# Performance work log

Hardware: AMD Instinct MI355X
Metric: run time of the kernel (lower is better)

Reference implementation:

```python
import jax, jax.numpy as jnp
import numpy as np

DIM = 512
HEADS = 8
HEAD_DIM = DIM // HEADS
SCALE = DIM ** (-0.5)  # note: original uses full dim, not head_dim


def setup_inputs() -> dict:
    key = jax.random.key(0)
    ks = jax.random.split(key, 7)
    B, N = 4, 2048
    x = jax.random.normal(ks[0], (B, N, DIM), dtype=jnp.float32)
    A_phi = jax.random.normal(ks[1], (B, N, N), dtype=jnp.float32)
    # parameters (torch Linear: y = x @ W.T + b)
    w_qkv = jax.random.normal(ks[2], (3 * DIM, DIM), dtype=jnp.float32) * (DIM ** -0.5)
    b_qkv = jax.random.normal(ks[3], (3 * DIM,), dtype=jnp.float32) * 0.02
    w_out = jax.random.normal(ks[4], (DIM, DIM), dtype=jnp.float32) * (DIM ** -0.5)
    b_out = jax.random.normal(ks[5], (DIM,), dtype=jnp.float32) * 0.02
    gamma = jnp.array(1.0, dtype=jnp.float32)
    return {"x": x, "A_phi": A_phi, "w_qkv": w_qkv, "b_qkv": b_qkv,
            "w_out": w_out, "b_out": b_out, "gamma": gamma}


def reference(x, A_phi, w_qkv, b_qkv, w_out, b_out, gamma):
    B, N, D = x.shape
    qkv = x @ w_qkv.T + b_qkv  # [B,N,3D]
    q, k, v = jnp.split(qkv, 3, axis=-1)
    def to_heads(t):
        return t.reshape(B, N, HEADS, HEAD_DIM).transpose(0, 2, 1, 3)  # [B,H,N,d]
    q, k, v = to_heads(q), to_heads(k), to_heads(v)
    attn = jnp.einsum('bhqd,bhkd->bhqk', q, k) * SCALE
    attn = attn + gamma * A_phi[:, None, :, :]
    attn = jax.nn.softmax(attn, axis=-1)
    out = jnp.einsum('bhqk,bhkd->bhqd', attn, v)
    out = out.transpose(0, 2, 1, 3).reshape(B, N, D)
    return out @ w_out.T + b_out
```

## Files before the change

### kernel.cpp

```cpp
#include <hip/hip_runtime.h>

#define NSEQ 2048
#define SCALE 0.04419417382415922f
#define LOG2E 1.44269504088896f

typedef __attribute__((ext_vector_type(8))) short short8v;
typedef __attribute__((ext_vector_type(4))) float f32x4;

#define GLOAD_LDS16(g, l) __builtin_amdgcn_global_load_lds( \
    (const __attribute__((address_space(1))) void*)(g),     \
    (__attribute__((address_space(3))) void*)(l), 16, 0, 0)

__device__ __forceinline__ unsigned short f2bf(float f) {
    unsigned int u = __builtin_bit_cast(unsigned int, f);
    u += 0x7fff + ((u >> 16) & 1);
    return (unsigned short)(u >> 16);
}

__device__ __forceinline__ float exp2_fast(float x) {
    float r; asm("v_exp_f32 %0, %1" : "=v"(r) : "v"(x)); return r;
}

__device__ __forceinline__ unsigned int pack_bf16_rh(float a, float b) {
    unsigned int ua = __builtin_bit_cast(unsigned int, a) + 0x8000u;
    unsigned int ub = __builtin_bit_cast(unsigned int, b) + 0x8000u;
    return __builtin_amdgcn_perm(ub, ua, 0x07060302u);
}

__global__ __launch_bounds__(256) void cvt_all(
    const float* __restrict__ x, const float* __restrict__ wq,
    const float* __restrict__ wo,
    unsigned short* __restrict__ xb, unsigned short* __restrict__ wqb,
    unsigned short* __restrict__ wob)
{
    int bid = blockIdx.x;
    const float* in;
    unsigned short* out;
    int i;
    if (bid < 4096)      { in = x;  out = xb;  i = bid * 256 + threadIdx.x; }
    else if (bid < 4864) { in = wq; out = wqb; i = (bid - 4096) * 256 + threadIdx.x; }
    else                 { in = wo; out = wob; i = (bid - 4864) * 256 + threadIdx.x; }
    float4 v = ((const float4*)in)[i];
    ushort4 o;
    o.x = f2bf(v.x); o.y = f2bf(v.y); o.z = f2bf(v.z); o.w = f2bf(v.w);
    ((ushort4*)out)[i] = o;
}

template<int MODE, int BM, int BN, int NX, int NWG>
__global__ __launch_bounds__(256) void gemm_bf16(
    const unsigned short* __restrict__ A,
    const unsigned short* __restrict__ W,
    const float* __restrict__ bias,
    unsigned short* __restrict__ Qws,
    unsigned short* __restrict__ Kws,
    unsigned short* __restrict__ Vtws,
    float* __restrict__ Cout)
{
    const int WM = BM / 2, WN = BN / 2;
    __shared__ __attribute__((aligned(16))) unsigned short As[BM * 64];
    __shared__ __attribute__((aligned(16))) unsigned short Bs[BN * 64];

    int tid = threadIdx.x;
    int lane = tid & 63, w = tid >> 6;
    int wm = w >> 1, wn = w & 1;
    int g = lane >> 4, fr = lane & 15;

    int id = blockIdx.x + NX * blockIdx.y;
    int wgid = (id & 7) * (NWG / 8) + (id >> 3);
    int m0 = (wgid / NX) * BM, n0 = (wgid % NX) * BN;

    f32x4 acc[WM / 16][4] = {};

    for (int k0 = 0; k0 < 512; k0 += 64) {
        __syncthreads();
#pragma unroll
        for (int c = 0; c < BM * 8 / 256; ++c) {
            int chunk = tid + c * 256;
            int row = chunk >> 3, c8 = chunk & 7;
            int gcol = (c8 ^ (row & 7)) * 8;
            GLOAD_LDS16(A + (size_t)(m0 + row) * 512 + k0 + gcol, &As[chunk * 8]);
        }
#pragma unroll
        for (int c = 0; c < BN * 8 / 256; ++c) {
            int chunk = tid + c * 256;
            int row = chunk >> 3, c8 = chunk & 7;
            int gcol = (c8 ^ (row & 7)) * 8;
            GLOAD_LDS16(W + (size_t)(n0 + row) * 512 + k0 + gcol, &Bs[chunk * 8]);
        }
        __syncthreads();
#pragma unroll
        for (int kk = 0; kk < 2; ++kk) {
            short8v af[WM / 16], bf[4];
#pragma unroll
            for (int mi = 0; mi < WM / 16; ++mi) {
                int row = wm * WM + mi * 16 + fr;
                af[mi] = *(const short8v*)(&As[row * 64 + (((kk * 4 + g) ^ (row & 7)) * 8)]);
            }
#pragma unroll
            for (int ni = 0; ni < 4; ++ni) {
                int row = wn * WN + ni * 16 + fr;
                bf[ni] = *(const short8v*)(&Bs[row * 64 + (((kk * 4 + g) ^ (row & 7)) * 8)]);
            }
#pragma unroll
            for (int mi = 0; mi < WM / 16; ++mi)
#pragma unroll
                for (int ni = 0; ni < 4; ++ni)
                    acc[mi][ni] = __builtin_amdgcn_mfma_f32_16x16x32_bf16(
                        af[mi], bf[ni], acc[mi][ni], 0, 0, 0);
        }
    }

#pragma unroll
    for (int mi = 0; mi < WM / 16; ++mi) {
#pragma unroll
        for (int ni = 0; ni < 4; ++ni) {
            int col = n0 + wn * WN + ni * 16 + fr;
            float bb = bias[col];
            int row0 = m0 + wm * WM + mi * 16 + g * 4;
            if (MODE == 0) {
                int b = row0 >> 11, s0 = row0 & 2047;
                if (col < 512) {
                    int h = col >> 6, d = col & 63;
#pragma unroll
                    for (int r = 0; r < 4; ++r)
                        Qws[(((size_t)(b * 8 + h) * NSEQ + s0 + r) << 6) + d] =
                            f2bf((acc[mi][ni][r] + bb) * (SCALE * LOG2E));
                } else if (col < 1024) {
                    int c2 = col - 512; int h = c2 >> 6, d = c2 & 63;
#pragma unroll
                    for (int r = 0; r < 4; ++r)
                        Kws[(((size_t)(b * 8 + h) * NSEQ + s0 + r) << 6) + d] =
                            f2bf(acc[mi][ni][r] + bb);
                } else {
                    int c2 = col - 1024; int h = c2 >> 6, d = c2 & 63;
                    uint2 pv;
                    pv.x = pack_bf16_rh(acc[mi][ni][0] + bb, acc[mi][ni][1] + bb);
                    pv.y = pack_bf16_rh(acc[mi][ni][2] + bb, acc[mi][ni][3] + bb);
                    *(uint2*)(&Vtws[((size_t)(b * 8 + h) * 64 + d) * NSEQ + s0]) = pv;
                }
            } else {
#pragma unroll
                for (int r = 0; r < 4; ++r)
                    Cout[(size_t)(row0 + r) * 512 + col] = acc[mi][ni][r] + bb;
            }
        }
    }
}

__global__ __launch_bounds__(512, 3) void attn_kernel(
    const unsigned short* __restrict__ Qws,
    const unsigned short* __restrict__ Kws,
    const unsigned short* __restrict__ Vtws,
    const float* __restrict__ A_phi,
    const float* __restrict__ gamma_p,
    unsigned short* __restrict__ Oout)
{
    __shared__ __attribute__((aligned(16))) unsigned short Ks[2][64 * 64];
    __shared__ __attribute__((aligned(16))) unsigned short Vts[2][64 * 64];
    __shared__ __attribute__((aligned(16))) unsigned short Pl[8][16 * 64];

    int tid = threadIdx.x, lane = tid & 63, w = tid >> 6;
    int g = lane >> 4, fr = lane & 15;

    int id = blockIdx.x;
    int b = (id & 7) >> 1, p = id & 1;
    int j = id >> 3;
    int h = j & 7;
    int qt = ((j >> 3) << 1) | p;
    int bh = b * 8 + h;
    int q0 = qt * 128 + w * 16;
    float g2 = gamma_p[0] * LOG2E;

    const unsigned short* Kb = Kws + (size_t)bh * NSEQ * 64;
    const unsigned short* Vb = Vtws + (size_t)bh * 64 * NSEQ;
    const float* Ap = A_phi + (size_t)b * NSEQ * NSEQ;

    short8v qf[2];
#pragma unroll
    for (int dc = 0; dc < 2; ++dc)
        qf[dc] = *(const short8v*)(Qws + ((size_t)bh * NSEQ + q0 + fr) * 64 + dc * 32 + g * 8);

    int c = tid;
    int krow = c >> 3;
    int kchunk = c & 7;
    int swK = (kchunk ^ ((krow >> 2) & 7)) * 8;
    int swV = (kchunk ^ (krow & 7)) * 8;
    int kcol = kchunk * 8;

    float l_lane[4] = {};
    f32x4 o_acc[4] = {};

    {
        short8v k0v = *(const short8v*)(Kb + c * 8);
        short8v v0v = *(const short8v*)(Vb + (size_t)krow * NSEQ + kcol);
        *(short8v*)(&Ks[0][krow * 64 + swK]) = k0v;
        *(short8v*)(&Vts[0][krow * 64 + swV]) = v0v;
    }
    __syncthreads();

    for (int kt = 0; kt < NSEQ / 64; ++kt) {
        int cur = kt & 1;

        short8v kreg, vreg;
        if (kt < NSEQ / 64 - 1) {
            kreg = *(const short8v*)(Kb + (kt + 1) * 4096 + c * 8);
            vreg = *(const short8v*)(Vb + (size_t)krow * NSEQ + (kt + 1) * 64 + kcol);
        }

        float4 av[4];
#pragma unroll
        for (int r = 0; r < 4; ++r)
            av[r] = *(const float4*)(Ap + (size_t)(q0 + g * 4 + r) * NSEQ + kt * 64 + 4 * fr);

        f32x4 sa[4] = {};
        __builtin_amdgcn_s_setprio(1);
#pragma unroll
        for (int kf = 0; kf < 4; ++kf) {
            int row = 4 * fr + kf;
#pragma unroll
            for (int dc = 0; dc < 2; ++dc) {
                short8v kfrag = *(const short8v*)(
                    &Ks[cur][row * 64 + (((dc * 4 + g) ^ ((row >> 2) & 7)) * 8)]);
                sa[kf] = __builtin_amdgcn_mfma_f32_16x16x32_bf16(qf[dc], kfrag, sa[kf], 0, 0, 0);
            }
        }
        __builtin_amdgcn_s_setprio(0);

#pragma unroll
        for (int r = 0; r < 4; ++r) {
            float e0 = exp2_fast(fmaf(g2, av[r].x, sa[0][r]));
            float e1 = exp2_fast(fmaf(g2, av[r].y, sa[1][r]));
            float e2 = exp2_fast(fmaf(g2, av[r].z, sa[2][r]));
            float e3 = exp2_fast(fmaf(g2, av[r].w, sa[3][r]));
            l_lane[r] += (e0 + e1) + (e2 + e3);
            int rp = g * 4 + r;
            uint2 pp;
            pp.x = pack_bf16_rh(e0, e1);
            pp.y = pack_bf16_rh(e2, e3);
            *(uint2*)(&Pl[w][rp * 64 + (((fr >> 1) ^ (rp & 7)) * 8) + (fr & 1) * 4]) = pp;
        }
        asm volatile("s_waitcnt lgkmcnt(0)" ::: "memory");

#pragma unroll
        for (int kc = 0; kc < 2; ++kc) {
            short8v pf = *(const short8v*)(
                &Pl[w][fr * 64 + (((kc * 4 + g) ^ (fr & 7)) * 8)]);
            __builtin_amdgcn_s_setprio(1);
#pragma unroll
            for (int nf = 0; nf < 4; ++nf) {
                int vrow = nf * 16 + fr;
                short8v vf = *(const short8v*)(
                    &Vts[cur][vrow * 64 + (((kc * 4 + g) ^ (vrow & 7)) * 8)]);
                o_acc[nf] = __builtin_amdgcn_mfma_f32_16x16x32_bf16(pf, vf, o_acc[nf], 0, 0, 0);
            }
            __builtin_amdgcn_s_setprio(0);
        }

        if (kt < NSEQ / 64 - 1) {
            *(short8v*)(&Ks[cur ^ 1][krow * 64 + swK]) = kreg;
            *(short8v*)(&Vts[cur ^ 1][krow * 64 + swV]) = vreg;
        }
        __syncthreads();
    }

#pragma unroll
    for (int r = 0; r < 4; ++r) {
        float l = l_lane[r];
        l += __shfl_xor(l, 1);
        l += __shfl_xor(l, 2);
        l += __shfl_xor(l, 4);
        l += __shfl_xor(l, 8);
        float inv = 1.0f / l;
        int qg = q0 + g * 4 + r;
#pragma unroll
        for (int nf = 0; nf < 4; ++nf)
            Oout[((size_t)b * NSEQ + qg) * 512 + h * 64 + nf * 16 + fr] =
                f2bf(o_acc[nf][r] * inv);
    }
}

extern "C" void kernel_launch(void* const* d_in, const int* in_sizes, int n_in,
                              void* d_out, int out_size, void* d_ws, size_t ws_size,
                              hipStream_t stream) {
    const float* x      = (const float*)d_in[0];
    const float* A_phi  = (const float*)d_in[1];
    const float* w_qkv  = (const float*)d_in[2];
    const float* b_qkv  = (const float*)d_in[3];
    const float* w_out  = (const float*)d_in[4];
    const float* b_out  = (const float*)d_in[5];
    const float* gamma  = (const float*)d_in[6];
    float* out = (float*)d_out;

    unsigned short* xb   = (unsigned short*)d_ws;
    unsigned short* wqb  = xb  + (size_t)8192 * 512;
    unsigned short* wob  = wqb + (size_t)1536 * 512;
    unsigned short* Qws  = wob + (size_t)512 * 512;
    unsigned short* Kws  = Qws + (size_t)4 * 8 * NSEQ * 64;
    unsigned short* Vtws = Kws + (size_t)4 * 8 * NSEQ * 64;
    unsigned short* Oat  = Vtws + (size_t)4 * 8 * NSEQ * 64;

    cvt_all<<<dim3(5120), dim3(256), 0, stream>>>(x, w_qkv, w_out, xb, wqb, wob);

    gemm_bf16<0, 128, 128, 12, 768><<<dim3(12, 64), dim3(256), 0, stream>>>(
        xb, wqb, b_qkv, Qws, Kws, Vtws, nullptr);

    attn_kernel<<<dim3(512), dim3(512), 0, stream>>>(
        Qws, Kws, Vtws, A_phi, gamma, Oat);

    gemm_bf16<1, 64, 128, 4, 512><<<dim3(4, 128), dim3(256), 0, stream>>>(
        Oat, wob, b_out, nullptr, nullptr, nullptr, out);
}
```

Measured before the change: 104.6 us.

## Split key range across two wave groups with 32-row query tiles per wave

```diff
diff --git a/kernel.cpp b/kernel.cpp
--- a/kernel.cpp
+++ b/kernel.cpp
@@ -147,7 +147,7 @@
     }
 }
 
-__global__ __launch_bounds__(512, 3) void attn_kernel(
+__global__ __launch_bounds__(512, 2) void attn_kernel(
     const unsigned short* __restrict__ Qws,
     const unsigned short* __restrict__ Kws,
     const unsigned short* __restrict__ Vtws,
@@ -155,12 +155,11 @@
     const float* __restrict__ gamma_p,
     unsigned short* __restrict__ Oout)
 {
-    __shared__ __attribute__((aligned(16))) unsigned short Ks[2][64 * 64];
-    __shared__ __attribute__((aligned(16))) unsigned short Vts[2][64 * 64];
-    __shared__ __attribute__((aligned(16))) unsigned short Pl[8][16 * 64];
+    __shared__ __attribute__((aligned(16))) unsigned short lds[32768];
 
     int tid = threadIdx.x, lane = tid & 63, w = tid >> 6;
     int g = lane >> 4, fr = lane & 15;
+    int G = w >> 2, wg = w & 3;
 
     int id = blockIdx.x;
     int b = (id & 7) >> 1, p = id & 1;
@@ -168,51 +167,63 @@
     int h = j & 7;
     int qt = ((j >> 3) << 1) | p;
     int bh = b * 8 + h;
-    int q0 = qt * 128 + w * 16;
+    int q0 = qt * 128 + wg * 32;
     float g2 = gamma_p[0] * LOG2E;
 
     const unsigned short* Kb = Kws + (size_t)bh * NSEQ * 64;
     const unsigned short* Vb = Vtws + (size_t)bh * 64 * NSEQ;
     const float* Ap = A_phi + (size_t)b * NSEQ * NSEQ;
 
-    short8v qf[2];
-#pragma unroll
-    for (int dc = 0; dc < 2; ++dc)
-        qf[dc] = *(const short8v*)(Qws + ((size_t)bh * NSEQ + q0 + fr) * 64 + dc * 32 + g * 8);
-
-    int c = tid;
-    int krow = c >> 3;
-    int kchunk = c & 7;
-    int swK = (kchunk ^ ((krow >> 2) & 7)) * 8;
-    int swV = (kchunk ^ (krow & 7)) * 8;
-    int kcol = kchunk * 8;
-
-    float l_lane[4] = {};
-    f32x4 o_acc[4] = {};
+    short8v qf[2][2];
+#pragma unroll
+    for (int qs = 0; qs < 2; ++qs)
+#pragma unroll
+        for (int dc = 0; dc < 2; ++dc)
+            qf[qs][dc] = *(const short8v*)(
+                Qws + ((size_t)bh * NSEQ + q0 + qs * 16 + fr) * 64 + dc * 32 + g * 8);
+
+    int cg = tid & 255;
+    int sr0 = cg >> 3, sc0 = cg & 7;
+    int sr1 = (cg + 256) >> 3, sc1 = cg & 7;
+    int swK0 = (sc0 ^ ((sr0 >> 2) & 7)) * 8, swK1 = (sc1 ^ ((sr1 >> 2) & 7)) * 8;
+    int swV0 = (sc0 ^ (sr0 & 7)) * 8,        swV1 = (sc1 ^ (sr1 & 7)) * 8;
+    unsigned short* KsG = &lds[G * 4096];
+    unsigned short* VsG = &lds[8192 + G * 4096];
+    unsigned short* Pw  = &lds[16384 + w * 2048];
+    int tile0 = G * 16;
+
+    float l_lane[2][4] = {};
+    f32x4 o_acc[2][4] = {};
 
     {
-        short8v k0v = *(const short8v*)(Kb + c * 8);
-        short8v v0v = *(const short8v*)(Vb + (size_t)krow * NSEQ + kcol);
-        *(short8v*)(&Ks[0][krow * 64 + swK]) = k0v;
-        *(short8v*)(&Vts[0][krow * 64 + swV]) = v0v;
+        short8v k0 = *(const short8v*)(Kb + tile0 * 4096 + cg * 8);
+        short8v k1 = *(const short8v*)(Kb + tile0 * 4096 + (cg + 256) * 8);
+        short8v v0 = *(const short8v*)(Vb + (size_t)sr0 * NSEQ + tile0 * 64 + sc0 * 8);
+        short8v v1 = *(const short8v*)(Vb + (size_t)sr1 * NSEQ + tile0 * 64 + sc1 * 8);
+        *(short8v*)(&KsG[sr0 * 64 + swK0]) = k0;
+        *(short8v*)(&KsG[sr1 * 64 + swK1]) = k1;
+        *(short8v*)(&VsG[sr0 * 64 + swV0]) = v0;
+        *(short8v*)(&VsG[sr1 * 64 + swV1]) = v1;
     }
     __syncthreads();
 
-    for (int kt = 0; kt < NSEQ / 64; ++kt) {
-        int cur = kt & 1;
-
-        short8v kreg, vreg;
-        if (kt < NSEQ / 64 - 1) {
-            kreg = *(const short8v*)(Kb + (kt + 1) * 4096 + c * 8);
-            vreg = *(const short8v*)(Vb + (size_t)krow * NSEQ + (kt + 1) * 64 + kcol);
-        }
-
-        float4 av[4];
+    for (int t = 0; t < 16; ++t) {
+        int tile = tile0 + t;
+
+        short8v k0r, k1r, v0r, v1r;
+        if (t < 15) {
+            k0r = *(const short8v*)(Kb + (tile + 1) * 4096 + cg * 8);
+            k1r = *(const short8v*)(Kb + (tile + 1) * 4096 + (cg + 256) * 8);
+            v0r = *(const short8v*)(Vb + (size_t)sr0 * NSEQ + (tile + 1) * 64 + sc0 * 8);
+            v1r = *(const short8v*)(Vb + (size_t)sr1 * NSEQ + (tile + 1) * 64 + sc1 * 8);
+        }
+
+        float4 av0[4];
 #pragma unroll
         for (int r = 0; r < 4; ++r)
-            av[r] = *(const float4*)(Ap + (size_t)(q0 + g * 4 + r) * NSEQ + kt * 64 + 4 * fr);
-
-        f32x4 sa[4] = {};
+            av0[r] = *(const float4*)(Ap + (size_t)(q0 + g * 4 + r) * NSEQ + tile * 64 + 4 * fr);
+
+        f32x4 sa[2][4] = {};
         __builtin_amdgcn_s_setprio(1);
 #pragma unroll
         for (int kf = 0; kf < 4; ++kf) {
@@ -220,62 +231,105 @@
 #pragma unroll
             for (int dc = 0; dc < 2; ++dc) {
                 short8v kfrag = *(const short8v*)(
-                    &Ks[cur][row * 64 + (((dc * 4 + g) ^ ((row >> 2) & 7)) * 8)]);
-                sa[kf] = __builtin_amdgcn_mfma_f32_16x16x32_bf16(qf[dc], kfrag, sa[kf], 0, 0, 0);
+                    &KsG[row * 64 + (((dc * 4 + g) ^ ((row >> 2) & 7)) * 8)]);
+                sa[0][kf] = __builtin_amdgcn_mfma_f32_16x16x32_bf16(qf[0][dc], kfrag, sa[0][kf], 0, 0, 0);
+                sa[1][kf] = __builtin_amdgcn_mfma_f32_16x16x32_bf16(qf[1][dc], kfrag, sa[1][kf], 0, 0, 0);
             }
         }
         __builtin_amdgcn_s_setprio(0);
 
-#pragma unroll
-        for (int r = 0; r < 4; ++r) {
-            float e0 = exp2_fast(fmaf(g2, av[r].x, sa[0][r]));
-            float e1 = exp2_fast(fmaf(g2, av[r].y, sa[1][r]));
-            float e2 = exp2_fast(fmaf(g2, av[r].z, sa[2][r]));
-            float e3 = exp2_fast(fmaf(g2, av[r].w, sa[3][r]));
-            l_lane[r] += (e0 + e1) + (e2 + e3);
-            int rp = g * 4 + r;
-            uint2 pp;
-            pp.x = pack_bf16_rh(e0, e1);
-            pp.y = pack_bf16_rh(e2, e3);
-            *(uint2*)(&Pl[w][rp * 64 + (((fr >> 1) ^ (rp & 7)) * 8) + (fr & 1) * 4]) = pp;
+        float4 av1[4];
+#pragma unroll
+        for (int r = 0; r < 4; ++r)
+            av1[r] = *(const float4*)(Ap + (size_t)(q0 + 16 + g * 4 + r) * NSEQ + tile * 64 + 4 * fr);
+
+#pragma unroll
+        for (int qs = 0; qs < 2; ++qs) {
+#pragma unroll
+            for (int r = 0; r < 4; ++r) {
+                float4 a = (qs == 0) ? av0[r] : av1[r];
+                float e0 = exp2_fast(fmaf(g2, a.x, sa[qs][0][r]));
+                float e1 = exp2_fast(fmaf(g2, a.y, sa[qs][1][r]));
+                float e2 = exp2_fast(fmaf(g2, a.z, sa[qs][2][r]));
+                float e3 = exp2_fast(fmaf(g2, a.w, sa[qs][3][r]));
+                l_lane[qs][r] += (e0 + e1) + (e2 + e3);
+                int rp = qs * 16 + g * 4 + r;
+                uint2 pp;
+                pp.x = pack_bf16_rh(e0, e1);
+                pp.y = pack_bf16_rh(e2, e3);
+                *(uint2*)(&Pw[rp * 64 + (((fr >> 1) ^ (rp & 7)) * 8) + (fr & 1) * 4]) = pp;
+            }
         }
         asm volatile("s_waitcnt lgkmcnt(0)" ::: "memory");
 
 #pragma unroll
         for (int kc = 0; kc < 2; ++kc) {
-            short8v pf = *(const short8v*)(
-                &Pl[w][fr * 64 + (((kc * 4 + g) ^ (fr & 7)) * 8)]);
+            short8v pf0 = *(const short8v*)(&Pw[fr * 64 + (((kc * 4 + g) ^ (fr & 7)) * 8)]);
+            short8v pf1 = *(const short8v*)(&Pw[(16 + fr) * 64 + (((kc * 4 + g) ^ (fr & 7)) * 8)]);
             __builtin_amdgcn_s_setprio(1);
 #pragma unroll
             for (int nf = 0; nf < 4; ++nf) {
                 int vrow = nf * 16 + fr;
                 short8v vf = *(const short8v*)(
-                    &Vts[cur][vrow * 64 + (((kc * 4 + g) ^ (vrow & 7)) * 8)]);
-                o_acc[nf] = __builtin_amdgcn_mfma_f32_16x16x32_bf16(pf, vf, o_acc[nf], 0, 0, 0);
+                    &VsG[vrow * 64 + (((kc * 4 + g) ^ (vrow & 7)) * 8)]);
+                o_acc[0][nf] = __builtin_amdgcn_mfma_f32_16x16x32_bf16(pf0, vf, o_acc[0][nf], 0, 0, 0);
+                o_acc[1][nf] = __builtin_amdgcn_mfma_f32_16x16x32_bf16(pf1, vf, o_acc[1][nf], 0, 0, 0);
             }
             __builtin_amdgcn_s_setprio(0);
         }
 
-        if (kt < NSEQ / 64 - 1) {
-            *(short8v*)(&Ks[cur ^ 1][krow * 64 + swK]) = kreg;
-            *(short8v*)(&Vts[cur ^ 1][krow * 64 + swV]) = vreg;
-        }
         __syncthreads();
-    }
-
-#pragma unroll
-    for (int r = 0; r < 4; ++r) {
-        float l = l_lane[r];
-        l += __shfl_xor(l, 1);
-        l += __shfl_xor(l, 2);
-        l += __shfl_xor(l, 4);
-        l += __shfl_xor(l, 8);
-        float inv = 1.0f / l;
-        int qg = q0 + g * 4 + r;
-#pragma unroll
-        for (int nf = 0; nf < 4; ++nf)
-            Oout[((size_t)b * NSEQ + qg) * 512 + h * 64 + nf * 16 + fr] =
-                f2bf(o_acc[nf][r] * inv);
+        if (t < 15) {
+            *(short8v*)(&KsG[sr0 * 64 + swK0]) = k0r;
+            *(short8v*)(&KsG[sr1 * 64 + swK1]) = k1r;
+            *(short8v*)(&VsG[sr0 * 64 + swV0]) = v0r;
+            *(short8v*)(&VsG[sr1 * 64 + swV1]) = v1r;
+        }
+        __syncthreads();
+    }
+
+    float lred[2][4];
+#pragma unroll
+    for (int qs = 0; qs < 2; ++qs)
+#pragma unroll
+        for (int r = 0; r < 4; ++r) {
+            float l = l_lane[qs][r];
+            l += __shfl_xor(l, 1);
+            l += __shfl_xor(l, 2);
+            l += __shfl_xor(l, 4);
+            l += __shfl_xor(l, 8);
+            lred[qs][r] = l;
+        }
+
+    float* Ob = (float*)&lds[0];
+    float* Lb = (float*)&lds[16384];
+    if (G == 1) {
+#pragma unroll
+        for (int qs = 0; qs < 2; ++qs)
+#pragma unroll
+            for (int r = 0; r < 4; ++r) {
+                int row = qs * 16 + g * 4 + r;
+#pragma unroll
+                for (int nf = 0; nf < 4; ++nf)
+                    Ob[(wg * 32 + row) * 64 + nf * 16 + fr] = o_acc[qs][nf][r];
+                if (fr == 0) Lb[wg * 32 + row] = lred[qs][r];
+            }
+    }
+    __syncthreads();
+    if (G == 0) {
+#pragma unroll
+        for (int qs = 0; qs < 2; ++qs)
+#pragma unroll
+            for (int r = 0; r < 4; ++r) {
+                int row = qs * 16 + g * 4 + r;
+                float inv = 1.0f / (lred[qs][r] + Lb[wg * 32 + row]);
+                int qg = q0 + row;
+#pragma unroll
+                for (int nf = 0; nf < 4; ++nf) {
+                    float val = (o_acc[qs][nf][r] + Ob[(wg * 32 + row) * 64 + nf * 16 + fr]) * inv;
+                    Oout[((size_t)b * NSEQ + qg) * 512 + h * 64 + nf * 16 + fr] = f2bf(val);
+                }
+            }
     }
 }
 
```

After: 116.3 us. 1.11x slower.
